# Optimization experiments

Measured on AMD Instinct MI355X. Metric: run time of the kernel, lower is better.

## Reference

```python
import jax, jax.numpy as jnp
import numpy as np

VOCAB, EMB, HID, OUT = 50257, 256, 512, 4
SEQ, BATCH = 512, 256


def setup_inputs() -> dict:
    key = jax.random.key(0)
    ks = jax.random.split(key, 8)
    text = jax.random.randint(ks[0], (SEQ, BATCH), 0, VOCAB, dtype=jnp.int64)
    s_e = 1.0  # torch Embedding default init is N(0,1)
    emb = jax.random.normal(ks[1], (VOCAB, EMB), dtype=jnp.float32) * s_e
    k_rnn = 1.0 / np.sqrt(HID)  # torch RNN init U(-1/sqrt(H), 1/sqrt(H))
    W_ih = jax.random.uniform(ks[2], (HID, EMB), jnp.float32, -k_rnn, k_rnn)
    W_hh = jax.random.uniform(ks[3], (HID, HID), jnp.float32, -k_rnn, k_rnn)
    b_ih = jax.random.uniform(ks[4], (HID,), jnp.float32, -k_rnn, k_rnn)
    b_hh = jax.random.uniform(ks[5], (HID,), jnp.float32, -k_rnn, k_rnn)
    k_fc = 1.0 / np.sqrt(HID)
    fc_w = jax.random.uniform(ks[6], (OUT, HID), jnp.float32, -k_fc, k_fc)
    fc_b = jax.random.uniform(ks[7], (OUT,), jnp.float32, -k_fc, k_fc)
    return {"text": text, "emb": emb, "W_ih": W_ih, "W_hh": W_hh,
            "b_ih": b_ih, "b_hh": b_hh, "fc_w": fc_w, "fc_b": fc_b}


def reference(text, emb, W_ih, W_hh, b_ih, b_hh, fc_w, fc_b):
    # embedding lookup: [S, B] -> [S, B, E]
    embedded = emb[text]
    # precompute input contribution for all timesteps: [S, B, H]
    x_proj = jnp.einsum('sbe,he->sbh', embedded, W_ih) + b_ih + b_hh

    def step(h, xp):
        h_new = jnp.tanh(xp + h @ W_hh.T)  # [B, H]
        return h_new, None

    h0 = jnp.zeros((text.shape[1], W_hh.shape[0]), dtype=embedded.dtype)
    h_last, _ = jax.lax.scan(step, h0, x_proj)
    # final linear head on last hidden state: [B, OUT]
    return h_last @ fc_w.T + fc_b
```

## Files before the change

### kernel.cpp

```cpp
#include <hip/hip_runtime.h>
#include <hip/hip_bf16.h>
#include <stdint.h>

#define SEQ   512
#define BATCH 256
#define EMBD  256
#define HID   512
#define OUTD  4

typedef float  f32x4 __attribute__((ext_vector_type(4)));
typedef short  s16x8 __attribute__((ext_vector_type(8)));
typedef __bf16 bf16x8 __attribute__((ext_vector_type(8)));

static __device__ __forceinline__ short f2bf(float f) {
    union { float f; uint32_t u; } v; v.f = f;
    uint32_t u = v.u;
    u += 0x7fffu + ((u >> 16) & 1u);
    return (short)(u >> 16);
}
static __device__ __forceinline__ float bf2f(short s) {
    union { uint32_t u; float f; } v;
    v.u = ((uint32_t)(uint16_t)s) << 16;
    return v.f;
}

static __device__ __forceinline__ f32x4 mfma_bf16(s16x8 a, s16x8 b, f32x4 c) {
    return __builtin_amdgcn_mfma_f32_16x16x32_bf16(
        __builtin_bit_cast(bf16x8, a), __builtin_bit_cast(bf16x8, b), c, 0, 0, 0);
}

static __device__ __forceinline__ s16x8 load_coherent_b128(const void* p) {
    s16x8 r;
    asm volatile("global_load_dwordx4 %0, %1, off sc0 sc1"
                 : "=v"(r) : "v"(p) : "memory");
    return r;
}
static __device__ __forceinline__ void store_coherent_b128(void* p, s16x8 v) {
    asm volatile("global_store_dwordx4 %0, %1, off sc0 sc1"
                 :: "v"(p), "v"(v) : "memory");
}
static __device__ __forceinline__ void wait_vm0() {
    asm volatile("s_waitcnt vmcnt(0)" ::: "memory");
    __builtin_amdgcn_sched_barrier(0);
}

static __device__ __forceinline__ size_t xp_pidx(int s, int b, int c) {
    const int w   = c >> 6, rem = c & 63;
    const int u   = w * 64 + (((rem & 15) >> 2) << 4) + (b & 15);
    return ((size_t)(s * 16 + (b >> 4)) * 512 + u) * 16
           + ((rem >> 4) << 2) + (rem & 3);
}

__global__ __launch_bounds__(512, 1)
void xproj_kernel(const int* __restrict__ text, const float* __restrict__ emb,
                  const float* __restrict__ W_ih, const float* __restrict__ b_ih,
                  const float* __restrict__ b_hh, short* __restrict__ xp) {
    extern __shared__ char lds[];
    char* As = lds;
    char* Bs = lds + 65536;

    const int t    = threadIdx.x;
    const int row0 = blockIdx.x * 128;
    const int col0 = blockIdx.y * 128;

    {
        const int r   = t >> 2;
        const int kc  = (t & 3) * 64;
        const int tok = text[row0 + r];
        const float* src = emb + (size_t)tok * EMBD + kc;
        #pragma unroll
        for (int u = 0; u < 64; u += 8) {
            f32x4 x0 = *(const f32x4*)(src + u);
            f32x4 x1 = *(const f32x4*)(src + u + 4);
            s16x8 pk;
            pk[0]=f2bf(x0.x); pk[1]=f2bf(x0.y); pk[2]=f2bf(x0.z); pk[3]=f2bf(x0.w);
            pk[4]=f2bf(x1.x); pk[5]=f2bf(x1.y); pk[6]=f2bf(x1.z); pk[7]=f2bf(x1.w);
            int byte = (r * 512 + (kc + u) * 2) ^ ((r & 7) << 4);
            *(s16x8*)(As + byte) = pk;
        }
    }
    {
        const int c  = t >> 2;
        const int kc = (t & 3) * 64;
        const float* src = W_ih + (size_t)(col0 + c) * EMBD + kc;
        #pragma unroll
        for (int u = 0; u < 64; u += 8) {
            f32x4 x0 = *(const f32x4*)(src + u);
            f32x4 x1 = *(const f32x4*)(src + u + 4);
            s16x8 pk;
            pk[0]=f2bf(x0.x); pk[1]=f2bf(x0.y); pk[2]=f2bf(x0.z); pk[3]=f2bf(x0.w);
            pk[4]=f2bf(x1.x); pk[5]=f2bf(x1.y); pk[6]=f2bf(x1.z); pk[7]=f2bf(x1.w);
            int byte = (c * 512 + (kc + u) * 2) ^ ((c & 7) << 4);
            *(s16x8*)(Bs + byte) = pk;
        }
    }
    __syncthreads();

    const int lane = t & 63;
    const int w    = t >> 6;
    const int wm   = w >> 2;
    const int wn   = w & 3;
    const int lr   = lane & 15;
    const int lk   = (lane >> 4) * 8;

    f32x4 acc[4][2] = {};
    #pragma unroll
    for (int kk = 0; kk < 8; ++kk) {
        s16x8 a[4], b[2];
        #pragma unroll
        for (int mt = 0; mt < 4; ++mt) {
            int r = wm * 64 + mt * 16 + lr;
            int byte = (r * 512 + (kk * 32 + lk) * 2) ^ ((r & 7) << 4);
            a[mt] = *(const s16x8*)(As + byte);
        }
        #pragma unroll
        for (int nt = 0; nt < 2; ++nt) {
            int c = wn * 32 + nt * 16 + lr;
            int byte = (c * 512 + (kk * 32 + lk) * 2) ^ ((c & 7) << 4);
            b[nt] = *(const s16x8*)(Bs + byte);
        }
        #pragma unroll
        for (int mt = 0; mt < 4; ++mt)
            #pragma unroll
            for (int nt = 0; nt < 2; ++nt)
                acc[mt][nt] = mfma_bf16(a[mt], b[nt], acc[mt][nt]);
    }

    #pragma unroll
    for (int nt = 0; nt < 2; ++nt) {
        const int c = col0 + wn * 32 + nt * 16 + lr;
        const float bias = b_ih[c] + b_hh[c];
        #pragma unroll
        for (int mt = 0; mt < 4; ++mt) {
            #pragma unroll
            for (int r4 = 0; r4 < 4; ++r4) {
                const int rr = row0 + wm * 64 + mt * 16 + (lane >> 4) * 4 + r4;
                xp[xp_pidx(rr >> 8, rr & 255, c)] = f2bf(acc[mt][nt][r4] + bias);
            }
        }
    }
}

__global__ __launch_bounds__(256, 1)
void rnn_kernel(const float* __restrict__ W_hh, const short* __restrict__ xp,
                const float* __restrict__ fc_w, const float* __restrict__ fc_b,
                short* __restrict__ hbuf, unsigned int* __restrict__ bar,
                float* __restrict__ out) {
    extern __shared__ char lds[];
    short* hstage = (short*)(lds + 131072);

    const int bid  = blockIdx.x;
    const int gi   = (bid & 7) + ((bid >> 5) << 3);
    const int gj   = (bid >> 3) & 3;
    const int t    = threadIdx.x;
    const int lane = t & 63;
    const int w    = t >> 6;
    const int row0 = gi * 16;
    const int col0 = gj * 128;

    {
        const int c  = t >> 1;
        const int k0 = (t & 1) * 256;
        const float* src = W_hh + (size_t)(col0 + c) * HID + k0;
        #pragma unroll 4
        for (int u = 0; u < 256; u += 8) {
            f32x4 x0 = *(const f32x4*)(src + u);
            f32x4 x1 = *(const f32x4*)(src + u + 4);
            s16x8 pk;
            pk[0]=f2bf(x0.x); pk[1]=f2bf(x0.y); pk[2]=f2bf(x0.z); pk[3]=f2bf(x0.w);
            pk[4]=f2bf(x1.x); pk[5]=f2bf(x1.y); pk[6]=f2bf(x1.z); pk[7]=f2bf(x1.w);
            int byte = (c * 1024 + (k0 + u) * 2) ^ ((c & 7) << 4);
            *(s16x8*)(lds + byte) = pk;
        }
    }
    __syncthreads();

    const int lr    = lane & 15;
    const int lkb   = (lane >> 4) * 16;
    const int arow  = row0 + lr;
    const int crow0 = row0 + (lane >> 4) * 4;
    unsigned int* mybar = bar + gi;

    int p = 0;
    for (int s = 0; s < SEQ; ++s) {
        f32x4 acc[2];
        #pragma unroll
        for (int nt = 0; nt < 2; ++nt) {
            const int c = col0 + w * 32 + nt * 16 + lr;
            #pragma unroll
            for (int r = 0; r < 4; ++r)
                acc[nt][r] = bf2f(xp[xp_pidx(s, crow0 + r, c)]);
        }

        if (s > 0) {
            if (t == 0) {
                const unsigned int target = 4u * (unsigned int)s;
                int guard = 0;
                while (__hip_atomic_load(mybar, __ATOMIC_RELAXED,
                                         __HIP_MEMORY_SCOPE_AGENT) < target) {
                    __builtin_amdgcn_s_sleep(1);
                    if (++guard > (1 << 27)) break;
                }
            }
            __syncthreads();
        }

        const short* hb   = hbuf + (size_t)p * (BATCH * HID);
        const char*  hrow = (const char*)(hb + (size_t)arow * HID);
        s16x8 areg[16];
        #pragma unroll
        for (int kk = 0; kk < 16; ++kk)
            areg[kk] = load_coherent_b128(hrow + kk * 64 + lkb);
        wait_vm0();

        const int cl0 = w * 32 + lr;
        const int cl1 = cl0 + 16;
        #pragma unroll
        for (int kk = 0; kk < 16; ++kk) {
            const int b0b = (cl0 * 1024 + kk * 64 + lkb) ^ ((cl0 & 7) << 4);
            const int b1b = (cl1 * 1024 + kk * 64 + lkb) ^ ((cl1 & 7) << 4);
            const s16x8 b0v = *(const s16x8*)(lds + b0b);
            const s16x8 b1v = *(const s16x8*)(lds + b1b);
            acc[0] = mfma_bf16(areg[kk], b0v, acc[0]);
            acc[1] = mfma_bf16(areg[kk], b1v, acc[1]);
        }

        #pragma unroll
        for (int nt = 0; nt < 2; ++nt) {
            const int cl = w * 32 + nt * 16 + lr;
            #pragma unroll
            for (int r = 0; r < 4; ++r)
                hstage[((crow0 - row0) + r) * 128 + cl] = f2bf(tanhf(acc[nt][r]));
        }
        __syncthreads();

        {
            const int rr = t >> 4, c8 = (t & 15) * 8;
            s16x8 v = *(const s16x8*)(hstage + rr * 128 + c8);
            short* hn = hbuf + (size_t)(p ^ 1) * (BATCH * HID)
                             + (size_t)(row0 + rr) * HID + (col0 + c8);
            store_coherent_b128(hn, v);
        }
        __syncthreads();

        if (t == 0)
            __hip_atomic_fetch_add(mybar, 1u, __ATOMIC_RELAXED,
                                   __HIP_MEMORY_SCOPE_AGENT);
        p ^= 1;
    }

    if (gj == 0) {
        if (t == 0) {
            int guard = 0;
            while (__hip_atomic_load(mybar, __ATOMIC_RELAXED,
                                     __HIP_MEMORY_SCOPE_AGENT) < 4u * SEQ) {
                __builtin_amdgcn_s_sleep(1);
                if (++guard > (1 << 27)) break;
            }
        }
        __syncthreads();

        const int i  = t >> 2;
        const int q  = t & 3;
        const int bl = i >> 2;
        const int o  = i & 3;
        const short* hb = hbuf + (size_t)p * (BATCH * HID)
                               + (size_t)(row0 + bl) * HID + q * 128;
        s16x8 hv[16];
        #pragma unroll
        for (int kk = 0; kk < 16; ++kk)
            hv[kk] = load_coherent_b128((const char*)hb + kk * 16);
        wait_vm0();
        float sum = 0.f;
        #pragma unroll
        for (int kk = 0; kk < 16; ++kk)
            #pragma unroll
            for (int j = 0; j < 8; ++j)
                sum += bf2f(hv[kk][j]) * fc_w[o * HID + q * 128 + kk * 8 + j];
        sum += __shfl_xor(sum, 1);
        sum += __shfl_xor(sum, 2);
        if (q == 0)
            out[(row0 + bl) * OUTD + o] = sum + fc_b[o];
    }
}

extern "C" void kernel_launch(void* const* d_in, const int* in_sizes, int n_in,
                              void* d_out, int out_size, void* d_ws, size_t ws_size,
                              hipStream_t stream) {
    (void)in_sizes; (void)n_in; (void)out_size;
    const int*   text = (const int*)  d_in[0];
    const float* emb  = (const float*)d_in[1];
    const float* W_ih = (const float*)d_in[2];
    const float* W_hh = (const float*)d_in[3];
    const float* b_ih = (const float*)d_in[4];
    const float* b_hh = (const float*)d_in[5];
    const float* fc_w = (const float*)d_in[6];
    const float* fc_b = (const float*)d_in[7];
    float* out = (float*)d_out;

    char* ws = (char*)d_ws;
    short*        hbuf = (short*)ws;
    unsigned int* bar  = (unsigned int*)(ws + (512 << 10));
    short*        xpbf = (short*)(ws + (1 << 20));
    const size_t xp_bytes = (size_t)SEQ * BATCH * HID * 2;
    const size_t need = ((size_t)1 << 20) + xp_bytes;
    if (ws_size < need) return;

    hipMemsetAsync(ws, 0, (512 << 10) + 4096, stream);

    hipFuncSetAttribute(reinterpret_cast<const void*>(&xproj_kernel),
                        hipFuncAttributeMaxDynamicSharedMemorySize, 131072);
    hipFuncSetAttribute(reinterpret_cast<const void*>(&rnn_kernel),
                        hipFuncAttributeMaxDynamicSharedMemorySize, 135168);
    xproj_kernel<<<dim3(1024, 4, 1), 512, 131072, stream>>>(
        text, emb, W_ih, b_ih, b_hh, xpbf);
    rnn_kernel<<<64, 256, 135168, stream>>>(
        W_hh, xpbf, fc_w, fc_b, hbuf, bar, out);
}
```

Before: 2.343 ms.

## Replace atomic counter barrier with per-block flag vector and repack xproj layout

Swaps the single atomic counter per batch group for four per-block step flags. Every thread polls all four with one 128-bit coherent load, which removes the thread-0 spin followed by __syncthreads. The x-projection output is reordered so each thread fetches its eight per-step values with one contiguous 16-byte load instead of eight scattered scalar loads. It also adds an explicit vmcnt wait before publishing the flag, and lowers the spin guard limit. Having every thread poll adds more polling traffic to global memory.

```diff
diff --git a/kernel.cpp b/kernel.cpp
--- a/kernel.cpp
+++ b/kernel.cpp
@@ -8,9 +8,10 @@
 #define HID   512
 #define OUTD  4
 
-typedef float  f32x4 __attribute__((ext_vector_type(4)));
-typedef short  s16x8 __attribute__((ext_vector_type(8)));
-typedef __bf16 bf16x8 __attribute__((ext_vector_type(8)));
+typedef float        f32x4 __attribute__((ext_vector_type(4)));
+typedef short        s16x8 __attribute__((ext_vector_type(8)));
+typedef unsigned int u32x4 __attribute__((ext_vector_type(4)));
+typedef __bf16       bf16x8 __attribute__((ext_vector_type(8)));
 
 static __device__ __forceinline__ short f2bf(float f) {
     union { float f; uint32_t u; } v; v.f = f;
@@ -39,16 +40,30 @@
     asm volatile("global_store_dwordx4 %0, %1, off sc0 sc1"
                  :: "v"(p), "v"(v) : "memory");
 }
+static __device__ __forceinline__ u32x4 load_flags_b128(const unsigned int* p) {
+    u32x4 r;
+    asm volatile("global_load_dwordx4 %0, %1, off sc0 sc1"
+                 : "=v"(r) : "v"(p) : "memory");
+    asm volatile("s_waitcnt vmcnt(0)" ::: "memory");
+    return r;
+}
+static __device__ __forceinline__ void store_flag(unsigned int* p, unsigned int v) {
+    asm volatile("global_store_dword %0, %1, off sc0 sc1"
+                 :: "v"(p), "v"(v) : "memory");
+}
 static __device__ __forceinline__ void wait_vm0() {
     asm volatile("s_waitcnt vmcnt(0)" ::: "memory");
     __builtin_amdgcn_sched_barrier(0);
 }
 
-static __device__ __forceinline__ size_t xp_pidx(int s, int b, int c) {
-    const int w   = c >> 6, rem = c & 63;
-    const int u   = w * 64 + (((rem & 15) >> 2) << 4) + (b & 15);
-    return ((size_t)(s * 16 + (b >> 4)) * 512 + u) * 16
-           + ((rem >> 4) << 2) + (rem & 3);
+static __device__ __forceinline__ size_t xp_pidx2(int s, int b, int c) {
+    const int gi  = b >> 4, gj = c >> 7;
+    const int bid = (gi & 7) | (gj << 3) | ((gi >> 3) << 5);
+    const int hi  = (b >> 2) & 3, r = b & 3;
+    const int c7  = c & 127;
+    const int w   = c7 >> 5, nt = (c7 >> 4) & 1, lr = c7 & 15;
+    const int tt  = w * 64 + hi * 16 + lr;
+    return (((size_t)(s * 64 + bid) * 256 + tt) << 3) + nt * 4 + r;
 }
 
 __global__ __launch_bounds__(512, 1)
@@ -135,7 +150,7 @@
             #pragma unroll
             for (int r4 = 0; r4 < 4; ++r4) {
                 const int rr = row0 + wm * 64 + mt * 16 + (lane >> 4) * 4 + r4;
-                xp[xp_pidx(rr >> 8, rr & 255, c)] = f2bf(acc[mt][nt][r4] + bias);
+                xp[xp_pidx2(rr >> 8, rr & 255, c)] = f2bf(acc[mt][nt][r4] + bias);
             }
         }
     }
@@ -179,30 +194,29 @@
     const int lkb   = (lane >> 4) * 16;
     const int arow  = row0 + lr;
     const int crow0 = row0 + (lane >> 4) * 4;
-    unsigned int* mybar = bar + gi;
+    unsigned int* gflags = bar + gi * 4;
 
     int p = 0;
     for (int s = 0; s < SEQ; ++s) {
+        const s16x8 xv = *(const s16x8*)(
+            xp + (((size_t)(s * 64 + bid) * 256 + t) << 3));
         f32x4 acc[2];
         #pragma unroll
-        for (int nt = 0; nt < 2; ++nt) {
-            const int c = col0 + w * 32 + nt * 16 + lr;
+        for (int nt = 0; nt < 2; ++nt)
             #pragma unroll
             for (int r = 0; r < 4; ++r)
-                acc[nt][r] = bf2f(xp[xp_pidx(s, crow0 + r, c)]);
-        }
+                acc[nt][r] = bf2f(xv[nt * 4 + r]);
 
         if (s > 0) {
-            if (t == 0) {
-                const unsigned int target = 4u * (unsigned int)s;
-                int guard = 0;
-                while (__hip_atomic_load(mybar, __ATOMIC_RELAXED,
-                                         __HIP_MEMORY_SCOPE_AGENT) < target) {
-                    __builtin_amdgcn_s_sleep(1);
-                    if (++guard > (1 << 27)) break;
-                }
+            const unsigned int target = (unsigned int)s;
+            int guard = 0;
+            for (;;) {
+                u32x4 f = load_flags_b128(gflags);
+                if (f.x >= target && f.y >= target &&
+                    f.z >= target && f.w >= target) break;
+                __builtin_amdgcn_s_sleep(1);
+                if (++guard > (1 << 22)) break;
             }
-            __syncthreads();
         }
 
         const short* hb   = hbuf + (size_t)p * (BATCH * HID);
@@ -241,24 +255,23 @@
                              + (size_t)(row0 + rr) * HID + (col0 + c8);
             store_coherent_b128(hn, v);
         }
+        wait_vm0();
         __syncthreads();
 
-        if (t == 0)
-            __hip_atomic_fetch_add(mybar, 1u, __ATOMIC_RELAXED,
-                                   __HIP_MEMORY_SCOPE_AGENT);
+        if (t == 0) store_flag(&bar[gi * 4 + gj], (unsigned int)(s + 1));
         p ^= 1;
     }
 
     if (gj == 0) {
-        if (t == 0) {
+        {
             int guard = 0;
-            while (__hip_atomic_load(mybar, __ATOMIC_RELAXED,
-                                     __HIP_MEMORY_SCOPE_AGENT) < 4u * SEQ) {
+            for (;;) {
+                u32x4 f = load_flags_b128(gflags);
+                if (f.x >= SEQ && f.y >= SEQ && f.z >= SEQ && f.w >= SEQ) break;
                 __builtin_amdgcn_s_sleep(1);
-                if (++guard > (1 << 27)) break;
+                if (++guard > (1 << 22)) break;
             }
         }
-        __syncthreads();
 
         const int i  = t >> 2;
         const int q  = t & 3;
```

Result: slower. 2.479 ms (+5.8%).
